# Performance work log

Hardware: AMD Instinct MI355X
Metric: run time of the kernel (lower is better)

Reference implementation:

```python
import jax, jax.numpy as jnp
import numpy as np

NUM_SAMPLES = 100  # hard-coded in the original forward


def _bilinear(img, x, y):
    """Bilinear sample img (H,W) at pixel coords x,y (any shape); border padding.
    Matches F.grid_sample(align_corners=True, padding_mode='border') since the
    original normalizes by (W-1)/(H-1) which maps back to the same pixel coords."""
    H, W = img.shape
    x0 = jnp.floor(x); y0 = jnp.floor(y)
    wx = x - x0; wy = y - y0
    x0i = jnp.clip(x0, 0, W - 1).astype(jnp.int32)
    x1i = jnp.clip(x0 + 1, 0, W - 1).astype(jnp.int32)
    y0i = jnp.clip(y0, 0, H - 1).astype(jnp.int32)
    y1i = jnp.clip(y0 + 1, 0, H - 1).astype(jnp.int32)
    return (img[y0i, x0i] * (1 - wx) * (1 - wy)
            + img[y0i, x1i] * wx * (1 - wy)
            + img[y1i, x0i] * (1 - wx) * wy
            + img[y1i, x1i] * wx * wy)


def setup_inputs() -> dict:
    key = jax.random.key(0)
    k1, k2, k3 = jax.random.split(key, 3)
    H = W = 2048
    N = 100000
    distance_image = jax.random.uniform(k1, (H, W), dtype=jnp.float32)
    points = jax.random.uniform(k2, (N, 2), dtype=jnp.float32) * (H - 1)
    normals = jax.random.normal(k3, (N, 2), dtype=jnp.float32)
    return {"distance_image": distance_image, "points": points, "normals": normals}


def reference(distance_image, points, normals):
    H, W = distance_image.shape
    N = points.shape[0]
    # original clamps both coords to [0, max(H-1, W-1)]
    pts = jnp.clip(points, 0.0, float(max(H - 1, W - 1)))  # (N,2)

    # direction perpendicular to normal, normalized
    d = jnp.stack([-normals[:, 1], normals[:, 0]], axis=-1)
    d = d / jnp.linalg.norm(d, axis=-1, keepdims=True)  # (N,2)
    dx, dy = d[:, 0], d[:, 1]
    px, py = pts[:, 0], pts[:, 1]

    maxf = jnp.finfo(d.dtype).max
    sdx = jnp.where(dx != 0, dx, 1.0)
    sdy = jnp.where(dy != 0, dy, 1.0)
    t_left = jnp.where(dx != 0, (0.0 - px) / sdx, -maxf)
    t_right = jnp.where(dx != 0, (W - 1.0 - px) / sdx, maxf)
    t_top = jnp.where(dy != 0, (0.0 - py) / sdy, -maxf)
    t_bottom = jnp.where(dy != 0, (H - 1.0 - py) / sdy, maxf)
    t_min = jnp.maximum(t_left, t_top)
    t_max = jnp.minimum(t_right, t_bottom)

    p1 = pts + t_min[:, None] * d  # (N,2)
    p2 = pts + t_max[:, None] * d  # (N,2)

    ts = jnp.linspace(0.0, 1.0, NUM_SAMPLES, dtype=pts.dtype)  # (S,)
    line = p1[:, None, :] + ts[None, :, None] * (p2 - p1)[:, None, :]  # (N,S,2)
    lx = jnp.clip(line[..., 0], 0.0, W - 1.0)
    ly = jnp.clip(line[..., 1], 0.0, H - 1.0)
    line = jnp.stack([lx, ly], axis=-1)  # clamped sampled points (N,S,2)

    vals = _bilinear(distance_image, lx, ly)  # (N,S)
    ref_val = _bilinear(distance_image, px, py)  # (N,)

    # local minima: strict minimum vs both neighbors, indices shifted by +1
    center = vals[:, 1:-1]
    minima = (center < vals[:, :-2]) & (center < vals[:, 2:])  # (N,S-2)

    # distance from each candidate (interior sample points) to the reference point
    dist = jnp.linalg.norm(line[:, 1:-1, :] - pts[:, None, :], axis=-1)  # (N,S-2)
    dist = jnp.where(minima, dist, jnp.inf)
    nearest = jnp.argmin(dist, axis=1)  # (N,)
    nearest_val = vals[jnp.arange(N), nearest + 1]  # (N,)

    # per-point mse of two scalars, then mean over points
    return jnp.mean((nearest_val - ref_val) ** 2)
```

## Files before the change

### kernel.cpp

```cpp
#include <hip/hip_runtime.h>
#include <float.h>
#include <math.h>

#define NSAMP 100
#define IMG_W 2048
#define IMG_H 2048

typedef _Float16 h2_t __attribute__((ext_vector_type(2), aligned(4)));
typedef _Float16 h4_t __attribute__((ext_vector_type(4), aligned(8)));
typedef _Float16 h8_t __attribute__((ext_vector_type(8), aligned(16)));

__global__ __launch_bounds__(256) void convert_kernel(const float* __restrict__ in,
                                                      h2_t* __restrict__ V,
                                                      double* __restrict__ accum,
                                                      unsigned int* __restrict__ done) {
    int idx = blockIdx.x * blockDim.x + threadIdx.x;
    if (idx == 0) { *accum = 0.0; *done = 0u; }
    int y  = idx >> 9;
    int x4 = (idx & 511) << 2;
    int y1 = min(y + 1, IMG_H - 1);
    float4 a = *(const float4*)(in + (size_t)y  * IMG_W + x4);
    float4 b = *(const float4*)(in + (size_t)y1 * IMG_W + x4);
    h8_t o;
    o[0] = (_Float16)a.x; o[1] = (_Float16)b.x;
    o[2] = (_Float16)a.y; o[3] = (_Float16)b.y;
    o[4] = (_Float16)a.z; o[5] = (_Float16)b.z;
    o[6] = (_Float16)a.w; o[7] = (_Float16)b.w;
    *(h8_t*)(V + (size_t)y * IMG_W + x4) = o;
}

__device__ __forceinline__ float bilinV(const h2_t* __restrict__ V, float x, float y) {
    float x0f = floorf(x), y0f = floorf(y);
    float wx = x - x0f, wy = y - y0f;
    int x0 = (int)x0f;
    int y0 = (int)y0f;
    int xa = min(x0, IMG_W - 2);
    bool edge = (x0 == IMG_W - 1);
    h4_t q = *(const h4_t*)(V + (size_t)y0 * IMG_W + xa);
    float v00 = edge ? (float)q[2] : (float)q[0];
    float v10 = edge ? (float)q[3] : (float)q[1];
    float v01 = (float)q[2];
    float v11 = (float)q[3];
    return v00 * (1.f - wx) * (1.f - wy) + v01 * wx * (1.f - wy)
         + v10 * (1.f - wx) * wy       + v11 * wx * wy;
}

__device__ __forceinline__ float tparam(int s) {
    return (s == NSAMP - 1) ? 1.0f : (float)((double)s * (1.0 / 99.0));
}

__global__ __launch_bounds__(256) void contour_loss_kernel(
        const h2_t* __restrict__ V,
        const float* __restrict__ points,
        const float* __restrict__ normals,
        double* __restrict__ accum,
        unsigned int* __restrict__ done,
        float* __restrict__ out,
        int N, int nblocks) {
    int i = blockIdx.x * blockDim.x + threadIdx.x;
    float sq = 0.f;
    if (i < N) {
        float px = fminf(fmaxf(points[2 * i],     0.f), 2047.f);
        float py = fminf(fmaxf(points[2 * i + 1], 0.f), 2047.f);
        float nx = normals[2 * i];
        float ny = normals[2 * i + 1];
        float ddx = -ny, ddy = nx;
        float nrm = sqrtf(ddx * ddx + ddy * ddy);
        float dx = ddx / nrm, dy = ddy / nrm;

        const float maxf = FLT_MAX;
        float sdx = (dx != 0.f) ? dx : 1.f;
        float sdy = (dy != 0.f) ? dy : 1.f;
        float t_left   = (dx != 0.f) ? (0.f    - px) / sdx : -maxf;
        float t_right  = (dx != 0.f) ? (2047.f - px) / sdx :  maxf;
        float t_top    = (dy != 0.f) ? (0.f    - py) / sdy : -maxf;
        float t_bottom = (dy != 0.f) ? (2047.f - py) / sdy :  maxf;
        float t_min = fmaxf(t_left, t_top);
        float t_max = fminf(t_right, t_bottom);

        float p1x = px + t_min * dx, p1y = py + t_min * dy;
        float p2x = px + t_max * dx, p2y = py + t_max * dy;
        float vx = p2x - p1x, vy = p2y - p1y;

        float ref_val = bilinV(V, px, py);

        float lx = fminf(fmaxf(p1x, 0.f), 2047.f);
        float ly = fminf(fmaxf(p1y, 0.f), 2047.f);
        float v_im1 = bilinV(V, lx, ly);
        float t1 = tparam(1);
        lx = fminf(fmaxf(p1x + t1 * vx, 0.f), 2047.f);
        ly = fminf(fmaxf(p1y + t1 * vy, 0.f), 2047.f);
        float v_i = bilinV(V, lx, ly);
        float cx = lx, cy = ly;

        float best_val = v_i;
        float best_d2  = INFINITY;

        #pragma unroll 8
        for (int s = 2; s < NSAMP; ++s) {
            float ts = tparam(s);
            float nlx = fminf(fmaxf(p1x + ts * vx, 0.f), 2047.f);
            float nly = fminf(fmaxf(p1y + ts * vy, 0.f), 2047.f);
            float v_ip1 = bilinV(V, nlx, nly);
            if (v_i < v_im1 && v_i < v_ip1) {
                float ex = cx - px, ey = cy - py;
                float d2 = ex * ex + ey * ey;
                if (d2 < best_d2) { best_d2 = d2; best_val = v_i; }
            }
            v_im1 = v_i; v_i = v_ip1; cx = nlx; cy = nly;
        }
        float diff = best_val - ref_val;
        sq = diff * diff;
    }

    for (int off = 32; off > 0; off >>= 1)
        sq += __shfl_down(sq, off);
    __shared__ float wsum[4];
    int lane = threadIdx.x & 63;
    int wid  = threadIdx.x >> 6;
    if (lane == 0) wsum[wid] = sq;
    __syncthreads();
    if (threadIdx.x == 0) {
        float bs = wsum[0] + wsum[1] + wsum[2] + wsum[3];
        atomicAdd(accum, (double)bs);
        __threadfence();
        unsigned int prev = atomicAdd(done, 1u);
        if (prev == (unsigned int)(nblocks - 1)) {
            double total = atomicAdd(accum, 0.0);
            out[0] = (float)(total / (double)N);
        }
    }
}

extern "C" void kernel_launch(void* const* d_in, const int* in_sizes, int n_in,
                              void* d_out, int out_size, void* d_ws, size_t ws_size,
                              hipStream_t stream) {
    const float* img     = (const float*)d_in[0];
    const float* points  = (const float*)d_in[1];
    const float* normals = (const float*)d_in[2];
    int N = in_sizes[1] / 2;
    float* out = (float*)d_out;

    char* ws = (char*)d_ws;
    h2_t* V = (h2_t*)ws;
    size_t off = (size_t)IMG_W * IMG_H * sizeof(h2_t);
    double* accum      = (double*)(ws + off);  off += 8;
    unsigned int* done = (unsigned int*)(ws + off);

    int conv_blocks = (IMG_W * IMG_H / 4) / 256;
    convert_kernel<<<conv_blocks, 256, 0, stream>>>(img, V, accum, done);

    int grid = (N + 255) / 256;
    contour_loss_kernel<<<grid, 256, 0, stream>>>(V, points, normals,
                                                  accum, done, out, N, grid);
}
```

Measured before the change: 128.9 us.

## Software-pipeline bilinear gathers in batches of ten with triple buffering

Restructures the per-point sampling loop into 10 batches of 10 samples. Loads for two batches ahead are issued into a triple-buffered register array before the current batch is interpolated and scanned for minima. The aim is to keep many independent global gathers in flight per thread and hide memory latency. It also vectorizes the point and normal loads into float2 and replaces the size_t row index with a 32-bit shift. The price is much higher register pressure (30 h4 values live at once), which can lower occupancy.

```diff
diff --git a/kernel.cpp b/kernel.cpp
--- a/kernel.cpp
+++ b/kernel.cpp
@@ -5,6 +5,8 @@
 #define NSAMP 100
 #define IMG_W 2048
 #define IMG_H 2048
+#define B   10
+#define NB  10
 
 typedef _Float16 h2_t __attribute__((ext_vector_type(2), aligned(4)));
 typedef _Float16 h4_t __attribute__((ext_vector_type(4), aligned(8)));
@@ -36,7 +38,7 @@
     int y0 = (int)y0f;
     int xa = min(x0, IMG_W - 2);
     bool edge = (x0 == IMG_W - 1);
-    h4_t q = *(const h4_t*)(V + (size_t)y0 * IMG_W + xa);
+    h4_t q = *(const h4_t*)(V + (y0 << 11) + xa);
     float v00 = edge ? (float)q[2] : (float)q[0];
     float v10 = edge ? (float)q[3] : (float)q[1];
     float v01 = (float)q[2];
@@ -60,11 +62,11 @@
     int i = blockIdx.x * blockDim.x + threadIdx.x;
     float sq = 0.f;
     if (i < N) {
-        float px = fminf(fmaxf(points[2 * i],     0.f), 2047.f);
-        float py = fminf(fmaxf(points[2 * i + 1], 0.f), 2047.f);
-        float nx = normals[2 * i];
-        float ny = normals[2 * i + 1];
-        float ddx = -ny, ddy = nx;
+        float2 pt = *(const float2*)(points  + 2 * (size_t)i);
+        float2 nm = *(const float2*)(normals + 2 * (size_t)i);
+        float px = fminf(fmaxf(pt.x, 0.f), 2047.f);
+        float py = fminf(fmaxf(pt.y, 0.f), 2047.f);
+        float ddx = -nm.y, ddy = nm.x;
         float nrm = sqrtf(ddx * ddx + ddy * ddy);
         float dx = ddx / nrm, dy = ddy / nrm;
 
@@ -84,31 +86,61 @@
 
         float ref_val = bilinV(V, px, py);
 
-        float lx = fminf(fmaxf(p1x, 0.f), 2047.f);
-        float ly = fminf(fmaxf(p1y, 0.f), 2047.f);
-        float v_im1 = bilinV(V, lx, ly);
-        float t1 = tparam(1);
-        lx = fminf(fmaxf(p1x + t1 * vx, 0.f), 2047.f);
-        ly = fminf(fmaxf(p1y + t1 * vy, 0.f), 2047.f);
-        float v_i = bilinV(V, lx, ly);
-        float cx = lx, cy = ly;
+        h4_t q[3][B];
 
-        float best_val = v_i;
+        auto issue = [&](int s, int buf, int j) {
+            float ts = tparam(s);
+            float lx = fminf(fmaxf(p1x + ts * vx, 0.f), 2047.f);
+            float ly = fminf(fmaxf(p1y + ts * vy, 0.f), 2047.f);
+            int x0 = (int)floorf(lx);
+            int y0 = (int)floorf(ly);
+            int xa = min(x0, IMG_W - 2);
+            q[buf][j] = *(const h4_t*)(V + (y0 << 11) + xa);
+        };
+
+        float vm1 = 0.f, v0 = 0.f, cx = 0.f, cy = 0.f;
+        float best_val = 0.f;
         float best_d2  = INFINITY;
 
-        #pragma unroll 8
-        for (int s = 2; s < NSAMP; ++s) {
+        auto process = [&](int s, int buf, int j) {
             float ts = tparam(s);
-            float nlx = fminf(fmaxf(p1x + ts * vx, 0.f), 2047.f);
-            float nly = fminf(fmaxf(p1y + ts * vy, 0.f), 2047.f);
-            float v_ip1 = bilinV(V, nlx, nly);
-            if (v_i < v_im1 && v_i < v_ip1) {
+            float lx = fminf(fmaxf(p1x + ts * vx, 0.f), 2047.f);
+            float ly = fminf(fmaxf(p1y + ts * vy, 0.f), 2047.f);
+            float x0f = floorf(lx), y0f = floorf(ly);
+            float wx = lx - x0f, wy = ly - y0f;
+            int x0 = (int)x0f;
+            bool edge = (x0 == IMG_W - 1);
+            h4_t qq = q[buf][j];
+            float v00 = edge ? (float)qq[2] : (float)qq[0];
+            float v10 = edge ? (float)qq[3] : (float)qq[1];
+            float v01 = (float)qq[2];
+            float v11 = (float)qq[3];
+            float vnew = v00 * (1.f - wx) * (1.f - wy) + v01 * wx * (1.f - wy)
+                       + v10 * (1.f - wx) * wy       + v11 * wx * wy;
+            if (s == 1) best_val = vnew;
+            if (s >= 2 && v0 < vm1 && v0 < vnew) {
                 float ex = cx - px, ey = cy - py;
                 float d2 = ex * ex + ey * ey;
-                if (d2 < best_d2) { best_d2 = d2; best_val = v_i; }
+                if (d2 < best_d2) { best_d2 = d2; best_val = v0; }
             }
-            v_im1 = v_i; v_i = v_ip1; cx = nlx; cy = nly;
+            vm1 = v0; v0 = vnew; cx = lx; cy = ly;
+        };
+
+        #pragma unroll
+        for (int j = 0; j < B; ++j) issue(j, 0, j);
+        #pragma unroll
+        for (int j = 0; j < B; ++j) issue(B + j, 1, j);
+
+        #pragma unroll
+        for (int b = 0; b < NB; ++b) {
+            if (b + 2 < NB) {
+                #pragma unroll
+                for (int j = 0; j < B; ++j) issue((b + 2) * B + j, (b + 2) % 3, j);
+            }
+            #pragma unroll
+            for (int j = 0; j < B; ++j) process(b * B + j, b % 3, j);
         }
+
         float diff = best_val - ref_val;
         sq = diff * diff;
     }
```

Result: slower. 138.7 us (+7.6%).
